# Optimization experiments

Measured on AMD Instinct MI355X. Metric: run time of the kernel, lower is better.

## Reference

```python
import jax, jax.numpy as jnp
import numpy as np

B, T = 1024, 512
BN_EPS = 1e-5


def _lstm_dir(x, w_ih, w_hh, b, reverse=False):
    """Single-direction LSTM, PyTorch gate order (i, f, g, o).
    x: [B, T, D]; w_ih: [4H, D]; w_hh: [4H, H]; b: [4H]. Returns [B, T, H]."""
    if reverse:
        x = x[:, ::-1]
    xw = jnp.einsum('btd,gd->btg', x, w_ih) + b  # precompute input contribution [B,T,4H]
    H = w_hh.shape[1]
    h0 = jnp.zeros((x.shape[0], H), x.dtype)

    def step(carry, xw_t):
        h, c = carry
        g = xw_t + h @ w_hh.T
        i, f, gg, o = jnp.split(g, 4, axis=-1)
        c = jax.nn.sigmoid(f) * c + jax.nn.sigmoid(i) * jnp.tanh(gg)
        h = jax.nn.sigmoid(o) * jnp.tanh(c)
        return (h, c), h

    _, ys = jax.lax.scan(step, (h0, h0), jnp.swapaxes(xw, 0, 1))
    ys = jnp.swapaxes(ys, 0, 1)  # [B,T,H]
    if reverse:
        ys = ys[:, ::-1]
    return ys


def _bilstm(x, w_ih, w_hh, b):
    # w_ih: [2,4H,D] (dir 0 = forward, dir 1 = backward)
    return jnp.concatenate([
        _lstm_dir(x, w_ih[0], w_hh[0], b[0]),
        _lstm_dir(x, w_ih[1], w_hh[1], b[1], reverse=True),
    ], axis=-1)


def _pool2(x):
    # MaxPool1d(2) over time on channel-last layout: [B,T,C] -> [B,T//2,C]
    b, t, c = x.shape
    return x.reshape(b, t // 2, 2, c).max(axis=2)


def setup_inputs() -> dict:
    key = jax.random.key(0)
    ks = iter(jax.random.split(key, 32))
    s = 0.1  # small init to avoid gate saturation
    d = {}
    d['x'] = jax.random.normal(next(ks), (B, 11, T), jnp.float32)
    d['conv_w'] = jax.random.normal(next(ks), (64, 11), jnp.float32) * s
    d['conv_b'] = jax.random.normal(next(ks), (64,), jnp.float32) * s
    d['bn_gamma'] = jax.random.uniform(next(ks), (64,), jnp.float32, 0.5, 1.5)
    d['bn_beta'] = jax.random.normal(next(ks), (64,), jnp.float32) * s
    d['bn_mean'] = jax.random.normal(next(ks), (64,), jnp.float32) * s
    d['bn_var'] = jax.random.uniform(next(ks), (64,), jnp.float32, 0.5, 1.5)
    for name, shp in [
        ('l1_wih0', (2, 64, 64)), ('l1_whh0', (2, 64, 16)), ('l1_b0', (2, 64)),
        ('l1_wih1', (2, 64, 32)), ('l1_whh1', (2, 64, 16)), ('l1_b1', (2, 64)),
        ('l2_wih0', (2, 32, 32)), ('l2_whh0', (2, 32, 8)), ('l2_b0', (2, 32)),
        ('l2_wih1', (2, 32, 16)), ('l2_whh1', (2, 32, 8)), ('l2_b1', (2, 32)),
        ('l3_wih0', (2, 16, 16)), ('l3_whh0', (2, 16, 4)), ('l3_b0', (2, 16)),
    ]:
        d[name] = jax.random.normal(next(ks), shp, jnp.float32) * s
    return d


def reference(x, conv_w, conv_b, bn_gamma, bn_beta, bn_mean, bn_var,
              l1_wih0, l1_whh0, l1_b0, l1_wih1, l1_whh1, l1_b1,
              l2_wih0, l2_whh0, l2_b0, l2_wih1, l2_whh1, l2_b1,
              l3_wih0, l3_whh0, l3_b0):
    # conv1x1: [B,11,T] -> [B,64,T]
    y = jnp.einsum('bct,oc->bot', x, conv_w) + conv_b[:, None]
    # BatchNorm1d (inference, running stats), fused scale/shift
    inv = bn_gamma / jnp.sqrt(bn_var + BN_EPS)
    y = (y - bn_mean[:, None]) * inv[:, None] + bn_beta[:, None]
    y = jnp.swapaxes(y, 1, 2)                      # [B,T,64]
    y = _bilstm(y, l1_wih0, l1_whh0, l1_b0)        # [B,T,32]
    y = _bilstm(y, l1_wih1, l1_whh1, l1_b1)        # [B,T,32]
    y = _pool2(y)                                  # [B,T/2,32]
    y = _bilstm(y, l2_wih0, l2_whh0, l2_b0)        # [B,T/2,16]
    y = _bilstm(y, l2_wih1, l2_whh1, l2_b1)        # [B,T/2,16]
    y = _pool2(y)                                  # [B,T/4,16]
    y = _bilstm(y, l3_wih0, l3_whh0, l3_b0)        # [B,T/4,8]
    return jnp.swapaxes(y, 1, 2)                   # [B,8,T/4]
```

## Files before the change

### kernel.cpp

```cpp
#include <hip/hip_runtime.h>

#define TB 128

typedef float v2f __attribute__((ext_vector_type(2)));
typedef _Float16 f16;
typedef _Float16 h2v __attribute__((ext_vector_type(2)));

__device__ __forceinline__ float rcp_f(float x) { return __builtin_amdgcn_rcpf(x); }
__device__ __forceinline__ float exp2_f(float x) { return __builtin_amdgcn_exp2f(x); }
__device__ __forceinline__ float dpp_xor2(float x) {
  return __int_as_float(__builtin_amdgcn_update_dpp(0, __float_as_int(x), 0x4E, 0xF, 0xF, true));
}
__device__ __forceinline__ float dpp_xor1(float x) {
  return __int_as_float(__builtin_amdgcn_update_dpp(0, __float_as_int(x), 0xB1, 0xF, 0xF, true));
}

#if __has_builtin(__builtin_amdgcn_fdot2)
__device__ __forceinline__ float fdot2(h2v a, h2v b, float c) {
  return __builtin_amdgcn_fdot2(a, b, c, false);
}
#else
__device__ __forceinline__ float fdot2(h2v a, h2v b, float c) {
  return fmaf((float)a.x, (float)b.x, fmaf((float)a.y, (float)b.y, c));
}
#endif

template<int D, int H, int T, int INS, int OUTS, int DEPTH, bool HIN,
         bool POOL, bool TOUT, typename OutT, typename InT>
__device__ __forceinline__ void scan(const void* wv, const float* hr,
                                     float bb, float am, float ab,
                                     const InT* in, OutT* out,
                                     int dir, int wl, float* h_base) {
  constexpr int NF4 = HIN ? (D / 8) : (D / 4);
  const int tau = wl & 3;
  const int j = (wl >> 2) & (H - 1);
  const bool st = (tau == 1) && ((wl >> 2) < H);
  if (wl < H) h_base[wl] = 0.f;
  __builtin_amdgcn_wave_barrier();

  int t = dir ? (T - 1) : 0;
  const int dt = dir ? -1 : 1;

  float4 bufs[DEPTH][NF4];
  auto ldin = [&](float4* dst, int tt) {
    tt = tt < 0 ? 0 : (tt > T - 1 ? T - 1 : tt);
    const float4* p = (const float4*)((const char*)in + (size_t)tt * INS * sizeof(InT));
#pragma unroll
    for (int i = 0; i < NF4; ++i) dst[i] = p[i];
  };
  auto xwdot = [&](const float4* b) -> float {
    if constexpr (HIN) {
      const h2v* hp = (const h2v*)b;
      const h2v* wh = (const h2v*)wv;
      float a0 = bb, a1 = 0.f, a2 = 0.f, a3 = 0.f;
#pragma unroll
      for (int i = 0; i < D / 2; i += 4) {
        a0 = fdot2(wh[i + 0], hp[i + 0], a0);
        a1 = fdot2(wh[i + 1], hp[i + 1], a1);
        a2 = fdot2(wh[i + 2], hp[i + 2], a2);
        a3 = fdot2(wh[i + 3], hp[i + 3], a3);
      }
      return (a0 + a1) + (a2 + a3);
    } else {
      const float* c = (const float*)b;
      const float* wr = (const float*)wv;
      v2f q0 = {bb, 0.f}, q1 = {0.f, 0.f};
#pragma unroll
      for (int i = 0; i < D; i += 4) {
        q0 = __builtin_elementwise_fma(*(const v2f*)(wr + i), *(const v2f*)(c + i), q0);
        q1 = __builtin_elementwise_fma(*(const v2f*)(wr + i + 2), *(const v2f*)(c + i + 2), q1);
      }
      v2f qs = q0 + q1;
      return qs.x + qs.y;
    }
  };

#pragma unroll
  for (int k = 0; k < DEPTH; ++k) ldin(bufs[k], t + k * dt);
  float xw = xwdot(bufs[0]);
  float cs = 0.f, pm = 0.f;

  for (int s = 0; s < T; s += DEPTH) {
#pragma unroll
    for (int k = 0; k < DEPTH; ++k) {
      v2f r0 = {xw, 0.f}, r1 = {0.f, 0.f};
#pragma unroll
      for (int i = 0; i < H; i += 4) {
        float4 h4 = *(const float4*)(h_base + i);
        r0 = __builtin_elementwise_fma(*(const v2f*)(hr + i), (v2f){h4.x, h4.y}, r0);
        r1 = __builtin_elementwise_fma(*(const v2f*)(hr + i + 2), (v2f){h4.z, h4.w}, r1);
      }
      v2f rs = r0 + r1;
      float acc = rs.x + rs.y;
      float sg = rcp_f(1.f + exp2_f(-acc));
      float a = fmaf(am, sg, ab);
      float b = dpp_xor2(a);
      float p = a * b;
      float q = dpp_xor1(p);
      float fv = (tau == 1) ? a : b;
      float ov = (tau == 1) ? b : a;
      cs = fmaf(fv, cs, q);
      float th = fmaf(2.f, rcp_f(1.f + exp2_f(-2.8853900818f * cs)), -1.f);
      float hv = ov * th;
      if (st) h_base[j] = hv;
      __builtin_amdgcn_wave_barrier();
      xw = xwdot(bufs[(k + 1) % DEPTH]);
      ldin(bufs[k], t + DEPTH * dt);
      if (st) {
        if constexpr (TOUT) {
          out[(dir * H + j) * T + t] = (OutT)hv;
        } else if constexpr (POOL) {
          if ((s + k) & 1) out[(t >> 1) * OUTS + dir * H + j] = (OutT)fmaxf(pm, hv);
          else pm = hv;
        } else {
          out[t * OUTS + dir * H + j] = (OutT)hv;
        }
      }
      t += dt;
    }
  }
}

template<int D, int H>
__device__ __forceinline__ void load_wbh(const float* __restrict__ wih,
                                         const float* __restrict__ whh,
                                         const float* __restrict__ bias,
                                         int dir, int wl,
                                         h2v* wh, float* hr, float& bb,
                                         float& am, float& ab) {
  constexpr float L2E = 1.4426950408889634f;
  const int tau = wl & 3;
  const int j = (wl >> 2) & (H - 1);
  const bool isg = (tau == 2);
  const float k = isg ? 2.f * L2E : L2E;
  am = isg ? 2.f : 1.f;
  ab = isg ? -1.f : 0.f;
  const int row = dir * 4 * H + tau * H + j;
  const float* p = wih + row * D;
#pragma unroll
  for (int i = 0; i < D / 2; ++i)
    wh[i] = (h2v){(f16)(p[2 * i] * k), (f16)(p[2 * i + 1] * k)};
  const float* q = whh + row * H;
#pragma unroll
  for (int i = 0; i < H; ++i) hr[i] = q[i] * k;
  bb = bias[row] * k;
}

__global__ __launch_bounds__(TB) void lstm_all(
    const float* __restrict__ x,
    const float* __restrict__ conv_w, const float* __restrict__ conv_b,
    const float* __restrict__ bn_g, const float* __restrict__ bn_b,
    const float* __restrict__ bn_m, const float* __restrict__ bn_v,
    const float* __restrict__ w1a_ih, const float* __restrict__ w1a_hh, const float* __restrict__ b1a,
    const float* __restrict__ w1b_ih, const float* __restrict__ w1b_hh, const float* __restrict__ b1b,
    const float* __restrict__ w2a_ih, const float* __restrict__ w2a_hh, const float* __restrict__ b2a,
    const float* __restrict__ w2b_ih, const float* __restrict__ w2b_hh, const float* __restrict__ b2b,
    const float* __restrict__ w3_ih, const float* __restrict__ w3_hh, const float* __restrict__ b3,
    float* __restrict__ out, f16* __restrict__ ws, int row0) {
  const int row = row0 + blockIdx.x;
  const int tid = threadIdx.x;
  const int wave = tid >> 6;
  const int lane = tid & 63;

  __shared__ __align__(16) char R1[24576];
  __shared__ __align__(16) f16 A2h[256 * 16];
  __shared__ __align__(16) float w2c[64][11];
  __shared__ float b2c[64];
  __shared__ __align__(16) float hb[32];

  float (*xs)[12] = (float(*)[12])R1;
  f16* LBh = (f16*)R1;
  f16* LB2h = (f16*)(R1 + 16384);
  f16* Ah = ws + (size_t)blockIdx.x * 16384;

  const float* xrow = x + (size_t)row * 5632;
  for (int i = tid; i < 5632; i += TB) {
    int c = i >> 9, t = i & 511;
    xs[t][c] = xrow[i];
  }
  for (int i = tid; i < 512; i += TB) xs[i][11] = 0.f;
  if (tid < 64) {
    float inv = bn_g[tid] * rsqrtf(bn_v[tid] + 1e-5f);
    for (int c = 0; c < 11; ++c) w2c[tid][c] = conv_w[tid * 11 + c] * inv;
    b2c[tid] = fmaf(conv_b[tid] - bn_m[tid], inv, bn_b[tid]);
  }
  __syncthreads();

  {
    constexpr float L2E = 1.4426950408889634f;
    const int tau = lane & 3;
    const int j = lane >> 2;
    const int row_l = wave * 64 + tau * 16 + j;
    float weff[12], beff;
#pragma unroll
    for (int c = 0; c < 12; ++c) weff[c] = 0.f;
    const float* wih = w1a_ih + row_l * 64;
    beff = b1a[row_l];
    for (int d = 0; d < 64; ++d) {
      float wd = wih[d];
      beff = fmaf(wd, b2c[d], beff);
#pragma unroll
      for (int c = 0; c < 11; ++c) weff[c] = fmaf(wd, w2c[d][c], weff[c]);
    }
    const bool isg = (tau == 2);
    const float k = isg ? 2.f * L2E : L2E;
#pragma unroll
    for (int c = 0; c < 12; ++c) weff[c] *= k;
    beff *= k;
    float am = isg ? 2.f : 1.f, ab = isg ? -1.f : 0.f;
    float hrw[16];
    const float* q = w1a_hh + row_l * 16;
#pragma unroll
    for (int i = 0; i < 16; ++i) hrw[i] = q[i] * k;
    scan<12, 16, 512, 12, 32, 2, false, false, false, f16, float>(
        weff, hrw, beff, am, ab, &xs[0][0], Ah, wave, lane, hb + wave * 16);
  }
  __syncthreads();

  {
    h2v wh[16]; float hr[16], bb, am, ab;
    load_wbh<32, 16>(w1b_ih, w1b_hh, b1b, wave, lane, wh, hr, bb, am, ab);
    scan<32, 16, 512, 32, 32, 4, true, true, false, f16, f16>(
        wh, hr, bb, am, ab, Ah, LBh, wave, lane, hb + wave * 16);
  }
  __syncthreads();

  if (wave == 0) {
    const int dir = lane >> 5, wl = lane & 31;
    h2v wh[16]; float hr[8], bb, am, ab;
    load_wbh<32, 8>(w2a_ih, w2a_hh, b2a, dir, wl, wh, hr, bb, am, ab);
    scan<32, 8, 256, 32, 16, 2, true, false, false, f16, f16>(
        wh, hr, bb, am, ab, LBh, A2h, dir, wl, hb + dir * 16);
  }
  __syncthreads();

  if (wave == 0) {
    const int dir = lane >> 5, wl = lane & 31;
    h2v wh[8]; float hr[8], bb, am, ab;
    load_wbh<16, 8>(w2b_ih, w2b_hh, b2b, dir, wl, wh, hr, bb, am, ab);
    scan<16, 8, 256, 16, 16, 2, true, true, false, f16, f16>(
        wh, hr, bb, am, ab, A2h, LB2h, dir, wl, hb + dir * 16);
  }
  __syncthreads();

  if (wave == 0) {
    const int dir = lane >> 5, wl = lane & 31;
    h2v wh[8]; float hr[4], bb, am, ab;
    load_wbh<16, 4>(w3_ih, w3_hh, b3, dir, wl, wh, hr, bb, am, ab);
    scan<16, 4, 128, 16, 8, 2, true, false, true, float, f16>(
        wh, hr, bb, am, ab, LB2h, out + (size_t)row * 1024, dir, wl, hb + dir * 16);
  }
}

extern "C" void kernel_launch(void* const* d_in, const int* in_sizes, int n_in,
                              void* d_out, int out_size, void* d_ws, size_t ws_size,
                              hipStream_t stream) {
  const float* x      = (const float*)d_in[0];
  const float* conv_w = (const float*)d_in[1];
  const float* conv_b = (const float*)d_in[2];
  const float* bn_g   = (const float*)d_in[3];
  const float* bn_b   = (const float*)d_in[4];
  const float* bn_m   = (const float*)d_in[5];
  const float* bn_v   = (const float*)d_in[6];
  const float* w1a_ih = (const float*)d_in[7];
  const float* w1a_hh = (const float*)d_in[8];
  const float* b1a    = (const float*)d_in[9];
  const float* w1b_ih = (const float*)d_in[10];
  const float* w1b_hh = (const float*)d_in[11];
  const float* b1b    = (const float*)d_in[12];
  const float* w2a_ih = (const float*)d_in[13];
  const float* w2a_hh = (const float*)d_in[14];
  const float* b2a    = (const float*)d_in[15];
  const float* w2b_ih = (const float*)d_in[16];
  const float* w2b_hh = (const float*)d_in[17];
  const float* b2b    = (const float*)d_in[18];
  const float* w3_ih  = (const float*)d_in[19];
  const float* w3_hh  = (const float*)d_in[20];
  const float* b3     = (const float*)d_in[21];

  const size_t per_row_bytes = 16384 * sizeof(f16);
  int rows_per = (int)(ws_size / per_row_bytes);
  if (rows_per < 1) rows_per = 1;
  if (rows_per > 1024) rows_per = 1024;

  for (int r0 = 0; r0 < 1024; r0 += rows_per) {
    int n = 1024 - r0;
    if (n > rows_per) n = rows_per;
    lstm_all<<<n, TB, 0, stream>>>(x, conv_w, conv_b, bn_g, bn_b, bn_m, bn_v,
                                   w1a_ih, w1a_hh, b1a, w1b_ih, w1b_hh, b1b,
                                   w2a_ih, w2a_hh, b2a, w2b_ih, w2b_hh, b2b,
                                   w3_ih, w3_hh, b3,
                                   (float*)d_out, (f16*)d_ws, r0);
  }
}
```

Before: 393.5 us.

## Broadcast LSTM hidden state via cross-lane DPP/permlane instead of LDS

Replaces the per-step write of the hidden state to shared memory, the wave barrier and the LDS reads with a register-only gather built from row-shift DPP and permlane16/32 swaps. Every lane keeps a full hidden vector, so the LDS round trip on the recurrent critical path goes away. The recurrent weights are permuted once at load time by running the same gather on lane indices, so each weight lines up with the lane order the gather produces. Gate combination is reworked so every lane holds h, not only the tau==1 lanes. The cost is more cross-lane instructions per step, plus a fallback that uses ds_swizzle or ds_bpermute when the permlane swap builtins are not available.

Measured after the change: 585.9 us. 48.9% more time.

```diff
diff --git a/kernel.cpp b/kernel.cpp
--- a/kernel.cpp
+++ b/kernel.cpp
@@ -8,11 +8,65 @@
 
 __device__ __forceinline__ float rcp_f(float x) { return __builtin_amdgcn_rcpf(x); }
 __device__ __forceinline__ float exp2_f(float x) { return __builtin_amdgcn_exp2f(x); }
-__device__ __forceinline__ float dpp_xor2(float x) {
-  return __int_as_float(__builtin_amdgcn_update_dpp(0, __float_as_int(x), 0x4E, 0xF, 0xF, true));
-}
-__device__ __forceinline__ float dpp_xor1(float x) {
-  return __int_as_float(__builtin_amdgcn_update_dpp(0, __float_as_int(x), 0xB1, 0xF, 0xF, true));
+
+template<int CTRL>
+__device__ __forceinline__ float dpp_f(float x) {
+  return __int_as_float(__builtin_amdgcn_update_dpp(0, __float_as_int(x), CTRL, 0xF, 0xF, true));
+}
+__device__ __forceinline__ float dpp_xor2(float x) { return dpp_f<0x4E>(x); }
+__device__ __forceinline__ float dpp_xor1(float x) { return dpp_f<0xB1>(x); }
+
+__device__ __forceinline__ void xchg16(float x, float& lo, float& hi) {
+#if __has_builtin(__builtin_amdgcn_permlane16_swap)
+  auto r = __builtin_amdgcn_permlane16_swap(__float_as_uint(x), __float_as_uint(x), false, false);
+  lo = __uint_as_float(r[0]);
+  hi = __uint_as_float(r[1]);
+#else
+  lo = x;
+  hi = __int_as_float(__builtin_amdgcn_ds_swizzle(__float_as_int(x), 0x401F));
+#endif
+}
+__device__ __forceinline__ void xchg32(float x, float& lo, float& hi) {
+#if __has_builtin(__builtin_amdgcn_permlane32_swap)
+  auto r = __builtin_amdgcn_permlane32_swap(__float_as_uint(x), __float_as_uint(x), false, false);
+  lo = __uint_as_float(r[0]);
+  hi = __uint_as_float(r[1]);
+#else
+  int la = ((int)(threadIdx.x & 63) ^ 32) << 2;
+  lo = x;
+  hi = __int_as_float(__builtin_amdgcn_ds_bpermute(la, __float_as_int(x)));
+#endif
+}
+
+template<int H>
+__device__ __forceinline__ void gather_h(float x, float* g) {
+  float a0 = x;
+  float a1 = dpp_f<0x124>(x);
+  float a2 = dpp_f<0x128>(x);
+  float a3 = dpp_f<0x12C>(x);
+  if constexpr (H == 4) {
+    g[0] = a0; g[1] = a1; g[2] = a2; g[3] = a3;
+  } else if constexpr (H == 8) {
+    xchg16(a0, g[0], g[1]); xchg16(a1, g[2], g[3]);
+    xchg16(a2, g[4], g[5]); xchg16(a3, g[6], g[7]);
+  } else {
+    float e0, o0, e1, o1, e2, o2, e3, o3;
+    xchg16(a0, e0, o0); xchg16(a1, e1, o1);
+    xchg16(a2, e2, o2); xchg16(a3, e3, o3);
+    xchg32(e0, g[0], g[1]);  xchg32(o0, g[2], g[3]);
+    xchg32(e1, g[4], g[5]);  xchg32(o1, g[6], g[7]);
+    xchg32(e2, g[8], g[9]);  xchg32(o2, g[10], g[11]);
+    xchg32(e3, g[12], g[13]); xchg32(o3, g[14], g[15]);
+  }
+}
+
+template<int H>
+__device__ __forceinline__ void calib_w(const float* __restrict__ whh_row,
+                                        float k, int j, float* wp) {
+  float g[H];
+  gather_h<H>((float)j, g);
+#pragma unroll
+  for (int m = 0; m < H; ++m) wp[m] = whh_row[(int)g[m]] * k;
 }
 
 #if __has_builtin(__builtin_amdgcn_fdot2)
@@ -27,16 +81,16 @@
 
 template<int D, int H, int T, int INS, int OUTS, int DEPTH, bool HIN,
          bool POOL, bool TOUT, typename OutT, typename InT>
-__device__ __forceinline__ void scan(const void* wv, const float* hr,
+__device__ __forceinline__ void scan(const void* wv, const float* wp,
                                      float bb, float am, float ab,
                                      const InT* in, OutT* out,
-                                     int dir, int wl, float* h_base) {
+                                     int dir, int wl) {
   constexpr int NF4 = HIN ? (D / 8) : (D / 4);
   const int tau = wl & 3;
   const int j = (wl >> 2) & (H - 1);
   const bool st = (tau == 1) && ((wl >> 2) < H);
-  if (wl < H) h_base[wl] = 0.f;
-  __builtin_amdgcn_wave_barrier();
+  const bool t1 = (tau & 1) != 0;
+  const bool t2 = (tau & 2) != 0;
 
   int t = dir ? (T - 1) : 0;
   const int dt = dir ? -1 : 1;
@@ -78,32 +132,34 @@
 #pragma unroll
   for (int k = 0; k < DEPTH; ++k) ldin(bufs[k], t + k * dt);
   float xw = xwdot(bufs[0]);
-  float cs = 0.f, pm = 0.f;
+  float hprev = 0.f, cs = 0.f, pm = 0.f;
 
   for (int s = 0; s < T; s += DEPTH) {
 #pragma unroll
     for (int k = 0; k < DEPTH; ++k) {
-      v2f r0 = {xw, 0.f}, r1 = {0.f, 0.f};
-#pragma unroll
-      for (int i = 0; i < H; i += 4) {
-        float4 h4 = *(const float4*)(h_base + i);
-        r0 = __builtin_elementwise_fma(*(const v2f*)(hr + i), (v2f){h4.x, h4.y}, r0);
-        r1 = __builtin_elementwise_fma(*(const v2f*)(hr + i + 2), (v2f){h4.z, h4.w}, r1);
+      float g[H];
+      gather_h<H>(hprev, g);
+      float a0 = xw, a1 = 0.f, a2 = 0.f, a3 = 0.f;
+#pragma unroll
+      for (int m = 0; m < H; m += 4) {
+        a0 = fmaf(wp[m + 0], g[m + 0], a0);
+        a1 = fmaf(wp[m + 1], g[m + 1], a1);
+        a2 = fmaf(wp[m + 2], g[m + 2], a2);
+        a3 = fmaf(wp[m + 3], g[m + 3], a3);
       }
-      v2f rs = r0 + r1;
-      float acc = rs.x + rs.y;
+      float acc = (a0 + a1) + (a2 + a3);
       float sg = rcp_f(1.f + exp2_f(-acc));
       float a = fmaf(am, sg, ab);
       float b = dpp_xor2(a);
-      float p = a * b;
-      float q = dpp_xor1(p);
-      float fv = (tau == 1) ? a : b;
-      float ov = (tau == 1) ? b : a;
-      cs = fmaf(fv, cs, q);
+      float e = dpp_xor1(a);
+      float d = dpp_xor1(b);
+      float ig = t1 ? e * d : a * b;
+      float fv = t1 ? (t2 ? b : a) : (t2 ? d : e);
+      float ov = t1 ? (t2 ? a : b) : (t2 ? e : d);
+      cs = fmaf(fv, cs, ig);
       float th = fmaf(2.f, rcp_f(1.f + exp2_f(-2.8853900818f * cs)), -1.f);
       float hv = ov * th;
-      if (st) h_base[j] = hv;
-      __builtin_amdgcn_wave_barrier();
+      hprev = hv;
       xw = xwdot(bufs[(k + 1) % DEPTH]);
       ldin(bufs[k], t + DEPTH * dt);
       if (st) {
@@ -126,7 +182,7 @@
                                          const float* __restrict__ whh,
                                          const float* __restrict__ bias,
                                          int dir, int wl,
-                                         h2v* wh, float* hr, float& bb,
+                                         h2v* wh, float* wp, float& bb,
                                          float& am, float& ab) {
   constexpr float L2E = 1.4426950408889634f;
   const int tau = wl & 3;
@@ -140,9 +196,7 @@
 #pragma unroll
   for (int i = 0; i < D / 2; ++i)
     wh[i] = (h2v){(f16)(p[2 * i] * k), (f16)(p[2 * i + 1] * k)};
-  const float* q = whh + row * H;
-#pragma unroll
-  for (int i = 0; i < H; ++i) hr[i] = q[i] * k;
+  calib_w<H>(whh + row * H, k, j, wp);
   bb = bias[row] * k;
 }
 
@@ -166,7 +220,6 @@
   __shared__ __align__(16) f16 A2h[256 * 16];
   __shared__ __align__(16) float w2c[64][11];
   __shared__ float b2c[64];
-  __shared__ __align__(16) float hb[32];
 
   float (*xs)[12] = (float(*)[12])R1;
   f16* LBh = (f16*)R1;
@@ -208,47 +261,45 @@
     for (int c = 0; c < 12; ++c) weff[c] *= k;
     beff *= k;
     float am = isg ? 2.f : 1.f, ab = isg ? -1.f : 0.f;
-    float hrw[16];
-    const float* q = w1a_hh + row_l * 16;
-#pragma unroll
-    for (int i = 0; i < 16; ++i) hrw[i] = q[i] * k;
+    float wp[16];
+    calib_w<16>(w1a_hh + row_l * 16, k, j, wp);
     scan<12, 16, 512, 12, 32, 2, false, false, false, f16, float>(
-        weff, hrw, beff, am, ab, &xs[0][0], Ah, wave, lane, hb + wave * 16);
+        weff, wp, beff, am, ab, &xs[0][0], Ah, wave, lane);
   }
   __syncthreads();
 
   {
-    h2v wh[16]; float hr[16], bb, am, ab;
-    load_wbh<32, 16>(w1b_ih, w1b_hh, b1b, wave, lane, wh, hr, bb, am, ab);
+    h2v wh[16]; float wp[16], bb, am, ab;
+    load_wbh<32, 16>(w1b_ih, w1b_hh, b1b, wave, lane, wh, wp, bb, am, ab);
     scan<32, 16, 512, 32, 32, 4, true, true, false, f16, f16>(
-        wh, hr, bb, am, ab, Ah, LBh, wave, lane, hb + wave * 16);
+        wh, wp, bb, am, ab, Ah, LBh, wave, lane);
   }
   __syncthreads();
 
   if (wave == 0) {
     const int dir = lane >> 5, wl = lane & 31;
-    h2v wh[16]; float hr[8], bb, am, ab;
-    load_wbh<32, 8>(w2a_ih, w2a_hh, b2a, dir, wl, wh, hr, bb, am, ab);
+    h2v wh[16]; float wp[8], bb, am, ab;
+    load_wbh<32, 8>(w2a_ih, w2a_hh, b2a, dir, wl, wh, wp, bb, am, ab);
     scan<32, 8, 256, 32, 16, 2, true, false, false, f16, f16>(
-        wh, hr, bb, am, ab, LBh, A2h, dir, wl, hb + dir * 16);
+        wh, wp, bb, am, ab, LBh, A2h, dir, wl);
   }
   __syncthreads();
 
   if (wave == 0) {
     const int dir = lane >> 5, wl = lane & 31;
-    h2v wh[8]; float hr[8], bb, am, ab;
-    load_wbh<16, 8>(w2b_ih, w2b_hh, b2b, dir, wl, wh, hr, bb, am, ab);
+    h2v wh[8]; float wp[8], bb, am, ab;
+    load_wbh<16, 8>(w2b_ih, w2b_hh, b2b, dir, wl, wh, wp, bb, am, ab);
     scan<16, 8, 256, 16, 16, 2, true, true, false, f16, f16>(
-        wh, hr, bb, am, ab, A2h, LB2h, dir, wl, hb + dir * 16);
+        wh, wp, bb, am, ab, A2h, LB2h, dir, wl);
   }
   __syncthreads();
 
   if (wave == 0) {
     const int dir = lane >> 5, wl = lane & 31;
-    h2v wh[8]; float hr[4], bb, am, ab;
-    load_wbh<16, 4>(w3_ih, w3_hh, b3, dir, wl, wh, hr, bb, am, ab);
+    h2v wh[8]; float wp[4], bb, am, ab;
+    load_wbh<16, 4>(w3_ih, w3_hh, b3, dir, wl, wh, wp, bb, am, ab);
     scan<16, 4, 128, 16, 8, 2, true, false, true, float, f16>(
-        wh, hr, bb, am, ab, LB2h, out + (size_t)row * 1024, dir, wl, hb + dir * 16);
+        wh, wp, bb, am, ab, LB2h, out + (size_t)row * 1024, dir, wl);
   }
 }
 
```

## Prefetch hidden state into registers and split small LSTM layers across both waves

Applied to the files above, without the earlier changes.

The scan loop now reloads the shared hidden state into registers right after the wave barrier, ahead of the input dot product and next-step input load. This lets LDS latency overlap other work instead of sitting on the recurrence critical path, at the cost of an extra barrier per step. The layer-2 and layer-3 scans now run one direction per wave across both waves, instead of packing both directions into wave 0 with the other wave idle. The wider lane mapping leaves many lanes masked for the small hidden sizes.

Result: slower. 406.8 us (+3.4%).

```diff
diff --git a/kernel.cpp b/kernel.cpp
--- a/kernel.cpp
+++ b/kernel.cpp
@@ -32,10 +32,15 @@
                                      const InT* in, OutT* out,
                                      int dir, int wl, float* h_base) {
   constexpr int NF4 = HIN ? (D / 8) : (D / 4);
+  constexpr int NH4 = H / 4;
   const int tau = wl & 3;
   const int j = (wl >> 2) & (H - 1);
   const bool st = (tau == 1) && ((wl >> 2) < H);
   if (wl < H) h_base[wl] = 0.f;
+  __builtin_amdgcn_wave_barrier();
+  float4 hreg[NH4];
+#pragma unroll
+  for (int i = 0; i < NH4; ++i) hreg[i] = *(const float4*)(h_base + 4 * i);
   __builtin_amdgcn_wave_barrier();
 
   int t = dir ? (T - 1) : 0;
@@ -85,10 +90,9 @@
     for (int k = 0; k < DEPTH; ++k) {
       v2f r0 = {xw, 0.f}, r1 = {0.f, 0.f};
 #pragma unroll
-      for (int i = 0; i < H; i += 4) {
-        float4 h4 = *(const float4*)(h_base + i);
-        r0 = __builtin_elementwise_fma(*(const v2f*)(hr + i), (v2f){h4.x, h4.y}, r0);
-        r1 = __builtin_elementwise_fma(*(const v2f*)(hr + i + 2), (v2f){h4.z, h4.w}, r1);
+      for (int i = 0; i < NH4; ++i) {
+        r0 = __builtin_elementwise_fma(*(const v2f*)(hr + 4 * i), (v2f){hreg[i].x, hreg[i].y}, r0);
+        r1 = __builtin_elementwise_fma(*(const v2f*)(hr + 4 * i + 2), (v2f){hreg[i].z, hreg[i].w}, r1);
       }
       v2f rs = r0 + r1;
       float acc = rs.x + rs.y;
@@ -104,6 +108,8 @@
       float hv = ov * th;
       if (st) h_base[j] = hv;
       __builtin_amdgcn_wave_barrier();
+#pragma unroll
+      for (int i = 0; i < NH4; ++i) hreg[i] = *(const float4*)(h_base + 4 * i);
       xw = xwdot(bufs[(k + 1) % DEPTH]);
       ldin(bufs[k], t + DEPTH * dt);
       if (st) {
@@ -116,6 +122,7 @@
           out[t * OUTS + dir * H + j] = (OutT)hv;
         }
       }
+      __builtin_amdgcn_wave_barrier();
       t += dt;
     }
   }
@@ -225,30 +232,27 @@
   }
   __syncthreads();
 
-  if (wave == 0) {
-    const int dir = lane >> 5, wl = lane & 31;
+  {
     h2v wh[16]; float hr[8], bb, am, ab;
-    load_wbh<32, 8>(w2a_ih, w2a_hh, b2a, dir, wl, wh, hr, bb, am, ab);
+    load_wbh<32, 8>(w2a_ih, w2a_hh, b2a, wave, lane, wh, hr, bb, am, ab);
     scan<32, 8, 256, 32, 16, 2, true, false, false, f16, f16>(
-        wh, hr, bb, am, ab, LBh, A2h, dir, wl, hb + dir * 16);
-  }
-  __syncthreads();
-
-  if (wave == 0) {
-    const int dir = lane >> 5, wl = lane & 31;
+        wh, hr, bb, am, ab, LBh, A2h, wave, lane, hb + wave * 16);
+  }
+  __syncthreads();
+
+  {
     h2v wh[8]; float hr[8], bb, am, ab;
-    load_wbh<16, 8>(w2b_ih, w2b_hh, b2b, dir, wl, wh, hr, bb, am, ab);
+    load_wbh<16, 8>(w2b_ih, w2b_hh, b2b, wave, lane, wh, hr, bb, am, ab);
     scan<16, 8, 256, 16, 16, 2, true, true, false, f16, f16>(
-        wh, hr, bb, am, ab, A2h, LB2h, dir, wl, hb + dir * 16);
-  }
-  __syncthreads();
-
-  if (wave == 0) {
-    const int dir = lane >> 5, wl = lane & 31;
+        wh, hr, bb, am, ab, A2h, LB2h, wave, lane, hb + wave * 16);
+  }
+  __syncthreads();
+
+  {
     h2v wh[8]; float hr[4], bb, am, ab;
-    load_wbh<16, 4>(w3_ih, w3_hh, b3, dir, wl, wh, hr, bb, am, ab);
+    load_wbh<16, 4>(w3_ih, w3_hh, b3, wave, lane, wh, hr, bb, am, ab);
     scan<16, 4, 128, 16, 8, 2, true, false, true, float, f16>(
-        wh, hr, bb, am, ab, LB2h, out + (size_t)row * 1024, dir, wl, hb + dir * 16);
+        wh, hr, bb, am, ab, LB2h, out + (size_t)row * 1024, wave, lane, hb + wave * 16);
   }
 }
 
```
